# Performance work log

Measured on AMD Instinct MI355X. Metric: run time of the kernel, lower is better.

The kernel has to match this reference:

```python
import jax, jax.numpy as jnp
import numpy as np

BN_EPS = 1e-5


def _maxpool2(x):
    # x: [b, c, h, w] -> [b, c, h//2, w//2], 2x2 max pool, stride 2
    b, c, h, w = x.shape
    return x.reshape(b, c, h // 2, 2, w // 2, 2).max(axis=(3, 5))


def setup_inputs() -> dict:
    key = jax.random.key(0)
    ks = jax.random.split(key, 9)
    b, C, H, W = 8, 512, 64, 64
    Ci = C // 2  # inter_channels = 256
    return {
        "x": jax.random.normal(ks[0], (b, C, H, W), dtype=jnp.float32),
        "g_w": jax.random.normal(ks[1], (Ci, C), dtype=jnp.float32) * 0.02,
        "g_b": jax.random.normal(ks[2], (Ci,), dtype=jnp.float32) * 0.02,
        "W_w": jax.random.normal(ks[3], (C, Ci), dtype=jnp.float32) * 0.02,
        "W_b": jax.random.normal(ks[4], (C,), dtype=jnp.float32) * 0.02,
        "bn_gamma": jax.random.normal(ks[5], (C,), dtype=jnp.float32),
        "bn_beta": jax.random.normal(ks[6], (C,), dtype=jnp.float32),
        "bn_mean": jax.random.normal(ks[7], (C,), dtype=jnp.float32),
        "bn_var": jax.random.uniform(ks[8], (C,), dtype=jnp.float32, minval=0.5, maxval=1.5),
    }


def reference(x, g_w, g_b, W_w, W_b, bn_gamma, bn_beta, bn_mean, bn_var):
    b, C, H, W = x.shape
    Ci = g_w.shape[0]

    # g branch: conv1x1 (C -> Ci) then 2x2 maxpool, flatten to values [b, Nk, Ci]
    g_x = jnp.einsum('bchw,oc->bohw', x, g_w) + g_b[None, :, None, None]
    g_x = _maxpool2(g_x).reshape(b, Ci, -1).transpose(0, 2, 1)  # [b, Nk, Ci]

    # theta: identity, flattened queries [b, Nq, C]
    theta = x.reshape(b, C, -1).transpose(0, 2, 1)  # [b, Nq, C]
    # phi: identity + 2x2 maxpool, keys [b, C, Nk]
    phi = _maxpool2(x).reshape(b, C, -1)  # [b, C, Nk]

    # attention (unscaled dot product + softmax over keys)
    f = jnp.einsum('bnc,bck->bnk', theta, phi)  # [b, Nq, Nk]
    attn = jax.nn.softmax(f, axis=-1)
    y = jnp.einsum('bnk,bko->bno', attn, g_x)  # [b, Nq, Ci]
    y = y.transpose(0, 2, 1).reshape(b, Ci, H, W)

    # W: conv1x1 (Ci -> C) + BatchNorm2d (eval mode with running stats)
    W_y = jnp.einsum('bchw,oc->bohw', y, W_w) + W_b[None, :, None, None]
    inv_std = jax.lax.rsqrt(bn_var + BN_EPS)
    W_y = (W_y - bn_mean[None, :, None, None]) * (bn_gamma * inv_std)[None, :, None, None] \
          + bn_beta[None, :, None, None]

    return W_y + x
```

## Files before the change

kernel.cpp:

```cpp
#include <hip/hip_runtime.h>
#include <stdint.h>

typedef __attribute__((ext_vector_type(4))) float f32x4;
typedef __attribute__((ext_vector_type(8))) short short8_t;
typedef __attribute__((ext_vector_type(8))) unsigned short ushort8_t;

__device__ __forceinline__ unsigned short f2bf(float f) {
    unsigned int u = __builtin_bit_cast(unsigned int, f);
    u = (u + 0x7fffu + ((u >> 16) & 1u)) >> 16;
    return (unsigned short)u;
}
__device__ __forceinline__ float bf2f(unsigned short h) {
    unsigned int u = ((unsigned int)h) << 16;
    return __builtin_bit_cast(float, u);
}

__device__ __forceinline__ void gll16(const unsigned short* g, unsigned short* l) {
    __builtin_amdgcn_global_load_lds(
        (const __attribute__((address_space(1))) void*)g,
        (__attribute__((address_space(3))) void*)l, 16, 0, 0);
}

__global__ __launch_bounds__(256) void prep_w(
    const float* __restrict__ g_w, const float* __restrict__ W_w,
    const float* __restrict__ W_b, const float* __restrict__ gamma,
    const float* __restrict__ beta, const float* __restrict__ mean,
    const float* __restrict__ var,
    unsigned short* __restrict__ gwb, unsigned short* __restrict__ wwb,
    float* __restrict__ bnA, float* __restrict__ bnB)
{
    int i = blockIdx.x * 256 + threadIdx.x;
    if (i < 256 * 512) { gwb[i] = f2bf(g_w[i]); wwb[i] = f2bf(W_w[i]); }
    if (i < 512) {
        float is = rsqrtf(var[i] + 1e-5f);
        float a = gamma[i] * is;
        bnA[i] = a;
        bnB[i] = (W_b[i] - mean[i]) * a + beta[i];
    }
}

__global__ void build_q(const float* __restrict__ x, unsigned short* __restrict__ Qh)
{
    __shared__ float t[32][33];
    int b = blockIdx.z, p0 = blockIdx.x * 32, c0 = blockIdx.y * 32;
    const float* xb = x + (long)b * 512 * 4096;
    int tx = threadIdx.x, ty = threadIdx.y;
    for (int i = 0; i < 4; i++)
        t[ty + i * 8][tx] = xb[(long)(c0 + ty + i * 8) * 4096 + p0 + tx];
    __syncthreads();
    unsigned short* qb = Qh + (long)b * 4096 * 512;
    for (int i = 0; i < 4; i++) {
        float v = t[tx][ty + i * 8];
        long row = (long)(p0 + ty + i * 8) * 512;
        qb[row + c0 + tx] = f2bf(v);
    }
}

__global__ void build_k(const float* __restrict__ x, unsigned short* __restrict__ Kh)
{
    __shared__ float t[32][33];
    int b = blockIdx.z, k0 = blockIdx.x * 32, c0 = blockIdx.y * 32;
    const float* xb = x + (long)b * 512 * 4096;
    int tx = threadIdx.x, ty = threadIdx.y;
    for (int i = 0; i < 4; i++) {
        int c = c0 + ty + i * 8;
        int k = k0 + tx;
        int h = k >> 5, w = k & 31;
        const float* base = xb + (long)c * 4096 + h * 128 + w * 2;
        float v = fmaxf(fmaxf(base[0], base[1]), fmaxf(base[64], base[65]));
        t[ty + i * 8][tx] = v;
    }
    __syncthreads();
    unsigned short* kb = Kh + (long)b * 1024 * 512;
    for (int i = 0; i < 4; i++) {
        float v = t[tx][ty + i * 8];
        long row = (long)(k0 + ty + i * 8) * 512;
        kb[row + c0 + tx] = f2bf(v);
    }
}

__global__ __launch_bounds__(256) void build_v(
    const unsigned short* __restrict__ Gt, const float* __restrict__ g_b,
    unsigned short* __restrict__ Gp)
{
    int b = blockIdx.z;
    int k  = blockIdx.x * 32 + (threadIdx.x & 31);
    int ci = blockIdx.y * 8 + (threadIdx.x >> 5);
    int h = k >> 5, w = k & 31;
    const unsigned short* g = Gt + (long)b * 4096 * 256;
    long p = (long)(h * 128 + w * 2) * 256 + ci;
    float v0 = bf2f(g[p]),        v1 = bf2f(g[p + 256]);
    float v2 = bf2f(g[p + 64*256]), v3 = bf2f(g[p + 65*256]);
    float v = fmaxf(fmaxf(v0, v1), fmaxf(v2, v3)) + g_b[ci];
    Gp[(long)b * 256 * 1024 + (long)ci * 1024 + k] = f2bf(v);
}

__global__ __launch_bounds__(256) void pv_fused(
    const unsigned short* __restrict__ S, long sbstr,
    const unsigned short* __restrict__ Gp, long gbstr,
    unsigned short* __restrict__ Y, long ybstr)
{
    __shared__ unsigned short lV[256 * 64];
    __shared__ unsigned short lP[64 * 64];
    __shared__ float pm[256], pl[256];
    __shared__ float lm[64], li[64];

    const int tid = threadIdx.x;
    const int wid = tid >> 6, lane = tid & 63;

    unsigned gx = gridDim.x, gy = gridDim.y;
    unsigned nwg = gx * gy;
    unsigned lin = blockIdx.x + gx * blockIdx.y;
    unsigned l = ((nwg & 7u) == 0u) ? ((lin & 7u) * (nwg >> 3) + (lin >> 3)) : lin;
    unsigned bx = l % gx, by = l / gx;

    const int q0 = (int)bx * 64;
    const unsigned short* Sb = S + by * sbstr + (long)q0 * 1024;
    const unsigned short* Gb = Gp + by * gbstr;
    unsigned short* Yb = Y + by * ybstr + (long)q0 * 256;

    {
        int r = tid >> 2, qq = tid & 3;
        const unsigned short* p = Sb + (long)r * 1024 + qq * 256;
        float m = -3.0e38f, s = 0.f;
        for (int i = 0; i < 32; i++) {
            ushort8_t v = *(const ushort8_t*)(p + i * 8);
            float f0 = bf2f(v[0]), f1 = bf2f(v[1]), f2 = bf2f(v[2]), f3 = bf2f(v[3]);
            float f4 = bf2f(v[4]), f5 = bf2f(v[5]), f6 = bf2f(v[6]), f7 = bf2f(v[7]);
            float cm = fmaxf(fmaxf(fmaxf(f0, f1), fmaxf(f2, f3)),
                             fmaxf(fmaxf(f4, f5), fmaxf(f6, f7)));
            if (cm > m) { s *= __expf(m - cm); m = cm; }
            s += __expf(f0 - m) + __expf(f1 - m) + __expf(f2 - m) + __expf(f3 - m)
               + __expf(f4 - m) + __expf(f5 - m) + __expf(f6 - m) + __expf(f7 - m);
        }
        pm[tid] = m; pl[tid] = s;
    }
    __syncthreads();
    if (tid < 64) {
        float m0 = pm[tid*4], m1 = pm[tid*4+1], m2 = pm[tid*4+2], m3 = pm[tid*4+3];
        float m = fmaxf(fmaxf(m0, m1), fmaxf(m2, m3));
        float s = pl[tid*4]   * __expf(m0 - m) + pl[tid*4+1] * __expf(m1 - m)
                + pl[tid*4+2] * __expf(m2 - m) + pl[tid*4+3] * __expf(m3 - m);
        lm[tid] = m; li[tid] = 1.0f / s;
    }

    const int wr = wid >> 1, wc = wid & 1;
    const int lr = lane & 15, lg = lane >> 4;
    const int srA = lane >> 3;
    const int scg = (((lane & 7) ^ srA) << 3);
    const int pr = tid >> 2;
    const int pc = (tid & 3) * 2;

    f32x4 acc[2][8];
    for (int mi = 0; mi < 2; mi++)
        for (int ni = 0; ni < 8; ni++)
            acc[mi][ni] = (f32x4){0.f, 0.f, 0.f, 0.f};

    for (int kb = 0; kb < 16; kb++) {
        __syncthreads();
        for (int i = 0; i < 8; i++) {
            int cibase = i * 32 + wid * 8;
            gll16(Gb + (long)(cibase + srA) * 1024 + kb * 64 + scg, &lV[cibase * 64]);
        }
        {
            float m = lm[pr];
            const unsigned short* sp = Sb + (long)pr * 1024 + kb * 64 + pc * 8;
            for (int j = 0; j < 2; j++) {
                ushort8_t v = *(const ushort8_t*)(sp + j * 8);
                ushort8_t o8;
                for (int e = 0; e < 8; e++) o8[e] = f2bf(__expf(bf2f(v[e]) - m));
                int c = pc + j;
                *(ushort8_t*)(&lP[pr * 64 + ((c ^ (pr & 7)) * 8)]) = o8;
            }
        }
        __syncthreads();
        for (int ks = 0; ks < 2; ks++) {
            short8_t af[2], bfr[8];
            for (int mi = 0; mi < 2; mi++) {
                int row = wr * 32 + mi * 16 + lr;
                int ch = ((ks * 4 + lg) ^ (row & 7)) * 8;
                af[mi] = *(const short8_t*)(&lP[row * 64 + ch]);
            }
            for (int ni = 0; ni < 8; ni++) {
                int row = wc * 128 + ni * 16 + lr;
                int ch = ((ks * 4 + lg) ^ (row & 7)) * 8;
                bfr[ni] = *(const short8_t*)(&lV[row * 64 + ch]);
            }
            for (int mi = 0; mi < 2; mi++)
                for (int ni = 0; ni < 8; ni++)
                    acc[mi][ni] = __builtin_amdgcn_mfma_f32_16x16x32_bf16(
                        af[mi], bfr[ni], acc[mi][ni], 0, 0, 0);
        }
    }

    for (int mi = 0; mi < 2; mi++) {
        for (int ni = 0; ni < 8; ni++) {
            int ci = wc * 128 + ni * 16 + lr;
            int rbase = wr * 32 + mi * 16 + lg * 4;
            for (int r = 0; r < 4; r++) {
                int row = rbase + r;
                Yb[(long)row * 256 + ci] = f2bf(acc[mi][ni][r] * li[row]);
            }
        }
    }
}

template<int EPI, int AFOLD, int BFOLD>
__global__ __launch_bounds__(256) void gemm_abt(
    const unsigned short* __restrict__ A, int lda, long abstr,
    const unsigned short* __restrict__ B, int ldb, long bbstr,
    void* __restrict__ Cv, int ldc, long cbstr,
    int K,
    const float* __restrict__ bnA, const float* __restrict__ bnB,
    const float* __restrict__ Xres, long xbstr)
{
    __shared__ unsigned short lA[128 * 64];
    __shared__ unsigned short lB[128 * 64];
    const int tid = threadIdx.x;
    const int wid = tid >> 6, lane = tid & 63;

    unsigned gx = gridDim.x, gy = gridDim.y;
    unsigned nwg = gx * gy * gridDim.z;
    unsigned lin = blockIdx.x + gx * (blockIdx.y + gy * blockIdx.z);
    unsigned l = ((nwg & 7u) == 0u) ? ((lin & 7u) * (nwg >> 3) + (lin >> 3)) : lin;
    unsigned bx = l % gx;
    unsigned rem = l / gx;
    unsigned by = rem % gy;
    unsigned bz = rem / gy;

    const int z = (int)bz;
    const int m0 = (int)by * 128, n0 = (int)bx * 128;
    const unsigned short* Ab = A + z * abstr;
    const unsigned short* Bb = B + z * bbstr;
    const int wr = wid >> 1, wc = wid & 1;
    const int lr = lane & 15, lg = lane >> 4;

    const int srA = lane >> 3;
    const int scg = (((lane & 7) ^ srA) << 3);

    f32x4 acc[4][4];
    for (int mi = 0; mi < 4; mi++)
        for (int ni = 0; ni < 4; ni++)
            acc[mi][ni] = (f32x4){0.f, 0.f, 0.f, 0.f};

    for (int k0 = 0; k0 < K; k0 += 64) {
        int ak0 = (AFOLD && k0 >= AFOLD) ? k0 - AFOLD : k0;
        int bk0 = (BFOLD && k0 >= BFOLD) ? k0 - BFOLD : k0;
        __syncthreads();
        for (int i = 0; i < 4; i++) {
            int rowbase = i * 32 + wid * 8;
            gll16(Ab + (long)(m0 + rowbase + srA) * lda + ak0 + scg, &lA[rowbase * 64]);
            gll16(Bb + (long)(n0 + rowbase + srA) * ldb + bk0 + scg, &lB[rowbase * 64]);
        }
        __syncthreads();
        for (int kk = 0; kk < 2; kk++) {
            short8_t af[4], bfr[4];
            for (int mi = 0; mi < 4; mi++) {
                int row = wr * 64 + mi * 16 + lr;
                int ch = ((kk * 4 + lg) ^ (row & 7)) * 8;
                af[mi] = *(const short8_t*)(&lA[row * 64 + ch]);
            }
            for (int ni = 0; ni < 4; ni++) {
                int row = wc * 64 + ni * 16 + lr;
                int ch = ((kk * 4 + lg) ^ (row & 7)) * 8;
                bfr[ni] = *(const short8_t*)(&lB[row * 64 + ch]);
            }
            for (int mi = 0; mi < 4; mi++)
                for (int ni = 0; ni < 4; ni++)
                    acc[mi][ni] = __builtin_amdgcn_mfma_f32_16x16x32_bf16(
                        af[mi], bfr[ni], acc[mi][ni], 0, 0, 0);
        }
    }

    for (int mi = 0; mi < 4; mi++) {
        for (int ni = 0; ni < 4; ni++) {
            int ncol = n0 + wc * 64 + ni * 16 + lr;
            int mrow = m0 + wr * 64 + mi * 16 + lg * 4;
            for (int r = 0; r < 4; r++) {
                int row = mrow + r;
                float v = acc[mi][ni][r];
                long idx = z * cbstr + (long)row * ldc + ncol;
                if (EPI == 0) {
                    ((float*)Cv)[idx] = v;
                } else if (EPI == 1) {
                    ((unsigned short*)Cv)[idx] = f2bf(v);
                } else {
                    float o = v * bnA[row] + bnB[row] + Xres[z * xbstr + (long)row * ldc + ncol];
                    ((float*)Cv)[idx] = o;
                }
            }
        }
    }
}

__global__ void copy_residual(const float* __restrict__ x, float* __restrict__ out, long n)
{
    for (long i = blockIdx.x * 256ll + threadIdx.x; i < n; i += (long)gridDim.x * 256)
        out[i] = x[i];
}

extern "C" void kernel_launch(void* const* d_in, const int* in_sizes, int n_in,
                              void* d_out, int out_size, void* d_ws, size_t ws_size,
                              hipStream_t stream)
{
    const float* x     = (const float*)d_in[0];
    const float* g_w   = (const float*)d_in[1];
    const float* g_b   = (const float*)d_in[2];
    const float* W_w   = (const float*)d_in[3];
    const float* W_b   = (const float*)d_in[4];
    const float* gamma = (const float*)d_in[5];
    const float* beta  = (const float*)d_in[6];
    const float* mean  = (const float*)d_in[7];
    const float* var   = (const float*)d_in[8];
    float* out = (float*)d_out;

    char* ws = (char*)d_ws;
    size_t o = 0;
    auto alloc = [&](size_t bytes) { size_t r = o; o = (o + bytes + 255) & ~(size_t)255; return r; };
    size_t o_gwb = alloc(256 * 512 * 2);
    size_t o_wwb = alloc(512 * 256 * 2);
    size_t o_bnA = alloc(512 * 4);
    size_t o_bnB = alloc(512 * 4);
    size_t o_q   = alloc(8ull * 4096 * 512 * 2);
    size_t o_k   = alloc(8ull * 1024 * 512 * 2);
    size_t o_gp  = alloc(8ull * 256 * 1024 * 2);
    size_t o_y   = alloc(8ull * 4096 * 256 * 2);
    size_t o_s   = o;
    const size_t srow_bytes = 1024ull * 2;
    const size_t sb1 = 4096ull * srow_bytes;

    int G = 0, RC = 0;
    if      (o_s + 8 * sb1 <= ws_size) G = 8;
    else if (o_s + 4 * sb1 <= ws_size) G = 4;
    else if (o_s + 2 * sb1 <= ws_size) G = 2;
    else if (o_s + 1 * sb1 <= ws_size) G = 1;
    else {
        for (int rc = 2048; rc >= 128; rc >>= 1)
            if (o_s + (size_t)rc * srow_bytes <= ws_size) { RC = rc; break; }
        if (!RC) {
            copy_residual<<<dim3(2048), dim3(256), 0, stream>>>(x, out, (long)out_size);
            return;
        }
    }

    unsigned short* gwb = (unsigned short*)(ws + o_gwb);
    unsigned short* wwb = (unsigned short*)(ws + o_wwb);
    float* bnA = (float*)(ws + o_bnA);
    float* bnB = (float*)(ws + o_bnB);
    unsigned short* Qh  = (unsigned short*)(ws + o_q);
    unsigned short* Kh  = (unsigned short*)(ws + o_k);
    unsigned short* Gp  = (unsigned short*)(ws + o_gp);
    unsigned short* Y   = (unsigned short*)(ws + o_y);
    unsigned short* S   = (unsigned short*)(ws + o_s);

    prep_w<<<dim3(512), dim3(256), 0, stream>>>(g_w, W_w, W_b, gamma, beta, mean, var,
                                                gwb, wwb, bnA, bnB);
    build_q<<<dim3(128, 16, 8), dim3(32, 8), 0, stream>>>(x, Qh);
    build_k<<<dim3(32, 16, 8), dim3(32, 8), 0, stream>>>(x, Kh);

    gemm_abt<1, 0, 0><<<dim3(2, 32, 8), dim3(256), 0, stream>>>(
        Qh, 512, 4096l * 512,
        gwb, 512, 0,
        (void*)Y, 256, 4096l * 256, 512,
        nullptr, nullptr, nullptr, 0);

    build_v<<<dim3(32, 32, 8), dim3(256), 0, stream>>>(Y, g_b, Gp);

    if (G) {
        for (int bg = 0; bg < 8; bg += G) {
            gemm_abt<1, 0, 0><<<dim3(8, 32, G), dim3(256), 0, stream>>>(
                Qh + (size_t)bg * 4096 * 512, 512, 4096l * 512,
                Kh + (size_t)bg * 1024 * 512, 512, 1024l * 512,
                (void*)S, 1024, 4096l * 1024, 512,
                nullptr, nullptr, nullptr, 0);
            pv_fused<<<dim3(64, G), dim3(256), 0, stream>>>(
                S, 4096l * 1024,
                Gp + (size_t)bg * 256 * 1024, 256l * 1024,
                Y + (size_t)bg * 4096 * 256, 4096l * 256);
        }
    } else {
        for (int b = 0; b < 8; b++) {
            for (int r0 = 0; r0 < 4096; r0 += RC) {
                const unsigned short* Aq = Qh + (size_t)b * 4096 * 512 + (size_t)r0 * 512;
                gemm_abt<1, 0, 0><<<dim3(8, RC / 128, 1), dim3(256), 0, stream>>>(
                    Aq, 512, 0,
                    Kh + (size_t)b * 1024 * 512, 512, 0,
                    (void*)S, 1024, 0, 512,
                    nullptr, nullptr, nullptr, 0);
                pv_fused<<<dim3(RC / 64, 1), dim3(256), 0, stream>>>(
                    S, 0,
                    Gp + (size_t)b * 256 * 1024, 0,
                    Y + ((size_t)b * 4096 + r0) * 256, 0);
            }
        }
    }

    gemm_abt<2, 0, 0><<<dim3(32, 4, 8), dim3(256), 0, stream>>>(
        wwb, 256, 0,
        Y, 256, 4096l * 256,
        (void*)out, 4096, 512l * 4096, 256,
        bnA, bnB, x, 512l * 4096);
}
```

Measured before the change: 195.2 us.

## Compute softmax row max in QK GEMM epilogue and fuse Q/K build kernels

The QK^T GEMM epilogue now writes per-tile row maxima (16 partials per row) to a workspace buffer. pv_fused reduces these to get the row max and accumulates the softmax denominator during its exp pass, which removes the separate full read of S for online max/sum statistics. build_q and build_k are merged into one kernel so x is read once for both the transpose and the pooled keys. The cost is an extra small buffer, some epilogue shuffles in the GEMM, and a shuffle reduction at the end of pv_fused.

```diff
diff --git a/kernel.cpp b/kernel.cpp
--- a/kernel.cpp
+++ b/kernel.cpp
@@ -39,43 +39,35 @@
     }
 }
 
-__global__ void build_q(const float* __restrict__ x, unsigned short* __restrict__ Qh)
-{
-    __shared__ float t[32][33];
-    int b = blockIdx.z, p0 = blockIdx.x * 32, c0 = blockIdx.y * 32;
+__global__ __launch_bounds__(256) void build_qk(
+    const float* __restrict__ x, unsigned short* __restrict__ Qh,
+    unsigned short* __restrict__ Kh)
+{
+    __shared__ float t[32][129];
+    int b = blockIdx.z;
+    int p0 = blockIdx.x * 128, c0 = blockIdx.y * 32;
     const float* xb = x + (long)b * 512 * 4096;
-    int tx = threadIdx.x, ty = threadIdx.y;
-    for (int i = 0; i < 4; i++)
-        t[ty + i * 8][tx] = xb[(long)(c0 + ty + i * 8) * 4096 + p0 + tx];
+    int tid = threadIdx.x;
+    for (int i = 0; i < 16; i++) {
+        int idx = i * 256 + tid;
+        int c = idx >> 7, p = idx & 127;
+        t[c][p] = xb[(long)(c0 + c) * 4096 + p0 + p];
+    }
     __syncthreads();
     unsigned short* qb = Qh + (long)b * 4096 * 512;
+    for (int i = 0; i < 16; i++) {
+        int idx = i * 256 + tid;
+        int p = idx >> 5, c = idx & 31;
+        qb[(long)(p0 + p) * 512 + c0 + c] = f2bf(t[c][p]);
+    }
+    unsigned short* kb = Kh + (long)b * 1024 * 512;
+    int kp0 = p0 >> 2;
     for (int i = 0; i < 4; i++) {
-        float v = t[tx][ty + i * 8];
-        long row = (long)(p0 + ty + i * 8) * 512;
-        qb[row + c0 + tx] = f2bf(v);
-    }
-}
-
-__global__ void build_k(const float* __restrict__ x, unsigned short* __restrict__ Kh)
-{
-    __shared__ float t[32][33];
-    int b = blockIdx.z, k0 = blockIdx.x * 32, c0 = blockIdx.y * 32;
-    const float* xb = x + (long)b * 512 * 4096;
-    int tx = threadIdx.x, ty = threadIdx.y;
-    for (int i = 0; i < 4; i++) {
-        int c = c0 + ty + i * 8;
-        int k = k0 + tx;
-        int h = k >> 5, w = k & 31;
-        const float* base = xb + (long)c * 4096 + h * 128 + w * 2;
-        float v = fmaxf(fmaxf(base[0], base[1]), fmaxf(base[64], base[65]));
-        t[ty + i * 8][tx] = v;
-    }
-    __syncthreads();
-    unsigned short* kb = Kh + (long)b * 1024 * 512;
-    for (int i = 0; i < 4; i++) {
-        float v = t[tx][ty + i * 8];
-        long row = (long)(k0 + ty + i * 8) * 512;
-        kb[row + c0 + tx] = f2bf(v);
+        int idx = i * 256 + tid;
+        int w = idx >> 5, c = idx & 31;
+        float v = fmaxf(fmaxf(t[c][2 * w], t[c][2 * w + 1]),
+                        fmaxf(t[c][64 + 2 * w], t[c][64 + 2 * w + 1]));
+        kb[(long)(kp0 + w) * 512 + c0 + c] = f2bf(v);
     }
 }
 
@@ -97,12 +89,12 @@
 
 __global__ __launch_bounds__(256) void pv_fused(
     const unsigned short* __restrict__ S, long sbstr,
+    const float* __restrict__ Mrow, long mbstr,
     const unsigned short* __restrict__ Gp, long gbstr,
     unsigned short* __restrict__ Y, long ybstr)
 {
     __shared__ unsigned short lV[256 * 64];
     __shared__ unsigned short lP[64 * 64];
-    __shared__ float pm[256], pl[256];
     __shared__ float lm[64], li[64];
 
     const int tid = threadIdx.x;
@@ -119,29 +111,11 @@
     const unsigned short* Gb = Gp + by * gbstr;
     unsigned short* Yb = Y + by * ybstr + (long)q0 * 256;
 
-    {
-        int r = tid >> 2, qq = tid & 3;
-        const unsigned short* p = Sb + (long)r * 1024 + qq * 256;
-        float m = -3.0e38f, s = 0.f;
-        for (int i = 0; i < 32; i++) {
-            ushort8_t v = *(const ushort8_t*)(p + i * 8);
-            float f0 = bf2f(v[0]), f1 = bf2f(v[1]), f2 = bf2f(v[2]), f3 = bf2f(v[3]);
-            float f4 = bf2f(v[4]), f5 = bf2f(v[5]), f6 = bf2f(v[6]), f7 = bf2f(v[7]);
-            float cm = fmaxf(fmaxf(fmaxf(f0, f1), fmaxf(f2, f3)),
-                             fmaxf(fmaxf(f4, f5), fmaxf(f6, f7)));
-            if (cm > m) { s *= __expf(m - cm); m = cm; }
-            s += __expf(f0 - m) + __expf(f1 - m) + __expf(f2 - m) + __expf(f3 - m)
-               + __expf(f4 - m) + __expf(f5 - m) + __expf(f6 - m) + __expf(f7 - m);
-        }
-        pm[tid] = m; pl[tid] = s;
-    }
-    __syncthreads();
     if (tid < 64) {
-        float m0 = pm[tid*4], m1 = pm[tid*4+1], m2 = pm[tid*4+2], m3 = pm[tid*4+3];
-        float m = fmaxf(fmaxf(m0, m1), fmaxf(m2, m3));
-        float s = pl[tid*4]   * __expf(m0 - m) + pl[tid*4+1] * __expf(m1 - m)
-                + pl[tid*4+2] * __expf(m2 - m) + pl[tid*4+3] * __expf(m3 - m);
-        lm[tid] = m; li[tid] = 1.0f / s;
+        const float* mr = Mrow + by * mbstr + (long)(q0 + tid) * 16;
+        float m = mr[0];
+        for (int j = 1; j < 16; j++) m = fmaxf(m, mr[j]);
+        lm[tid] = m;
     }
 
     const int wr = wid >> 1, wc = wid & 1;
@@ -155,6 +129,7 @@
     for (int mi = 0; mi < 2; mi++)
         for (int ni = 0; ni < 8; ni++)
             acc[mi][ni] = (f32x4){0.f, 0.f, 0.f, 0.f};
+    float psum = 0.f;
 
     for (int kb = 0; kb < 16; kb++) {
         __syncthreads();
@@ -168,7 +143,11 @@
             for (int j = 0; j < 2; j++) {
                 ushort8_t v = *(const ushort8_t*)(sp + j * 8);
                 ushort8_t o8;
-                for (int e = 0; e < 8; e++) o8[e] = f2bf(__expf(bf2f(v[e]) - m));
+                for (int e = 0; e < 8; e++) {
+                    float pe = __expf(bf2f(v[e]) - m);
+                    psum += pe;
+                    o8[e] = f2bf(pe);
+                }
                 int c = pc + j;
                 *(ushort8_t*)(&lP[pr * 64 + ((c ^ (pr & 7)) * 8)]) = o8;
             }
@@ -193,6 +172,11 @@
         }
     }
 
+    psum += __shfl_xor(psum, 1);
+    psum += __shfl_xor(psum, 2);
+    if ((tid & 3) == 0) li[pr] = 1.0f / psum;
+    __syncthreads();
+
     for (int mi = 0; mi < 2; mi++) {
         for (int ni = 0; ni < 8; ni++) {
             int ci = wc * 128 + ni * 16 + lr;
@@ -205,14 +189,15 @@
     }
 }
 
-template<int EPI, int AFOLD, int BFOLD>
+template<int EPI, int ROWMAX>
 __global__ __launch_bounds__(256) void gemm_abt(
     const unsigned short* __restrict__ A, int lda, long abstr,
     const unsigned short* __restrict__ B, int ldb, long bbstr,
     void* __restrict__ Cv, int ldc, long cbstr,
     int K,
     const float* __restrict__ bnA, const float* __restrict__ bnB,
-    const float* __restrict__ Xres, long xbstr)
+    const float* __restrict__ Xres, long xbstr,
+    float* __restrict__ Mrow, long mbstr)
 {
     __shared__ unsigned short lA[128 * 64];
     __shared__ unsigned short lB[128 * 64];
@@ -244,13 +229,11 @@
             acc[mi][ni] = (f32x4){0.f, 0.f, 0.f, 0.f};
 
     for (int k0 = 0; k0 < K; k0 += 64) {
-        int ak0 = (AFOLD && k0 >= AFOLD) ? k0 - AFOLD : k0;
-        int bk0 = (BFOLD && k0 >= BFOLD) ? k0 - BFOLD : k0;
         __syncthreads();
         for (int i = 0; i < 4; i++) {
             int rowbase = i * 32 + wid * 8;
-            gll16(Ab + (long)(m0 + rowbase + srA) * lda + ak0 + scg, &lA[rowbase * 64]);
-            gll16(Bb + (long)(n0 + rowbase + srA) * ldb + bk0 + scg, &lB[rowbase * 64]);
+            gll16(Ab + (long)(m0 + rowbase + srA) * lda + k0 + scg, &lA[rowbase * 64]);
+            gll16(Bb + (long)(n0 + rowbase + srA) * ldb + k0 + scg, &lB[rowbase * 64]);
         }
         __syncthreads();
         for (int kk = 0; kk < 2; kk++) {
@@ -269,6 +252,23 @@
                 for (int ni = 0; ni < 4; ni++)
                     acc[mi][ni] = __builtin_amdgcn_mfma_f32_16x16x32_bf16(
                         af[mi], bfr[ni], acc[mi][ni], 0, 0, 0);
+        }
+    }
+
+    if (ROWMAX) {
+        for (int mi = 0; mi < 4; mi++) {
+            for (int r = 0; r < 4; r++) {
+                float mx = fmaxf(fmaxf(acc[mi][0][r], acc[mi][1][r]),
+                                 fmaxf(acc[mi][2][r], acc[mi][3][r]));
+                mx = fmaxf(mx, __shfl_xor(mx, 1));
+                mx = fmaxf(mx, __shfl_xor(mx, 2));
+                mx = fmaxf(mx, __shfl_xor(mx, 4));
+                mx = fmaxf(mx, __shfl_xor(mx, 8));
+                if (lr == 0) {
+                    int row = m0 + wr * 64 + mi * 16 + lg * 4 + r;
+                    Mrow[z * mbstr + (long)row * 16 + bx * 2 + wc] = mx;
+                }
+            }
         }
     }
 
@@ -325,6 +325,7 @@
     size_t o_k   = alloc(8ull * 1024 * 512 * 2);
     size_t o_gp  = alloc(8ull * 256 * 1024 * 2);
     size_t o_y   = alloc(8ull * 4096 * 256 * 2);
+    size_t o_m   = alloc(8ull * 4096 * 16 * 4);
     size_t o_s   = o;
     const size_t srow_bytes = 1024ull * 2;
     const size_t sb1 = 4096ull * srow_bytes;
@@ -351,30 +352,32 @@
     unsigned short* Kh  = (unsigned short*)(ws + o_k);
     unsigned short* Gp  = (unsigned short*)(ws + o_gp);
     unsigned short* Y   = (unsigned short*)(ws + o_y);
+    float* Mrow         = (float*)(ws + o_m);
     unsigned short* S   = (unsigned short*)(ws + o_s);
 
     prep_w<<<dim3(512), dim3(256), 0, stream>>>(g_w, W_w, W_b, gamma, beta, mean, var,
                                                 gwb, wwb, bnA, bnB);
-    build_q<<<dim3(128, 16, 8), dim3(32, 8), 0, stream>>>(x, Qh);
-    build_k<<<dim3(32, 16, 8), dim3(32, 8), 0, stream>>>(x, Kh);
-
-    gemm_abt<1, 0, 0><<<dim3(2, 32, 8), dim3(256), 0, stream>>>(
+    build_qk<<<dim3(32, 16, 8), dim3(256), 0, stream>>>(x, Qh, Kh);
+
+    gemm_abt<1, 0><<<dim3(2, 32, 8), dim3(256), 0, stream>>>(
         Qh, 512, 4096l * 512,
         gwb, 512, 0,
         (void*)Y, 256, 4096l * 256, 512,
-        nullptr, nullptr, nullptr, 0);
+        nullptr, nullptr, nullptr, 0, nullptr, 0);
 
     build_v<<<dim3(32, 32, 8), dim3(256), 0, stream>>>(Y, g_b, Gp);
 
     if (G) {
         for (int bg = 0; bg < 8; bg += G) {
-            gemm_abt<1, 0, 0><<<dim3(8, 32, G), dim3(256), 0, stream>>>(
+            gemm_abt<1, 1><<<dim3(8, 32, G), dim3(256), 0, stream>>>(
                 Qh + (size_t)bg * 4096 * 512, 512, 4096l * 512,
                 Kh + (size_t)bg * 1024 * 512, 512, 1024l * 512,
                 (void*)S, 1024, 4096l * 1024, 512,
-                nullptr, nullptr, nullptr, 0);
+                nullptr, nullptr, nullptr, 0,
+                Mrow + (size_t)bg * 4096 * 16, 4096l * 16);
             pv_fused<<<dim3(64, G), dim3(256), 0, stream>>>(
                 S, 4096l * 1024,
+                Mrow + (size_t)bg * 4096 * 16, 4096l * 16,
                 Gp + (size_t)bg * 256 * 1024, 256l * 1024,
                 Y + (size_t)bg * 4096 * 256, 4096l * 256);
         }
@@ -382,22 +385,25 @@
         for (int b = 0; b < 8; b++) {
             for (int r0 = 0; r0 < 4096; r0 += RC) {
                 const unsigned short* Aq = Qh + (size_t)b * 4096 * 512 + (size_t)r0 * 512;
-                gemm_abt<1, 0, 0><<<dim3(8, RC / 128, 1), dim3(256), 0, stream>>>(
+                gemm_abt<1, 1><<<dim3(8, RC / 128, 1), dim3(256), 0, stream>>>(
                     Aq, 512, 0,
                     Kh + (size_t)b * 1024 * 512, 512, 0,
                     (void*)S, 1024, 0, 512,
-                    nullptr, nullptr, nullptr, 0);
+                    nullptr, nullptr, nullptr, 0,
+                    Mrow, 0);
                 pv_fused<<<dim3(RC / 64, 1), dim3(256), 0, stream>>>(
                     S, 0,
+                    Mrow, 0,
                     Gp + (size_t)b * 256 * 1024, 0,
                     Y + ((size_t)b * 4096 + r0) * 256, 0);
             }
         }
     }
 
-    gemm_abt<2, 0, 0><<<dim3(32, 4, 8), dim3(256), 0, stream>>>(
+    gemm_abt<2, 0><<<dim3(32, 4, 8), dim3(256), 0, stream>>>(
         wwb, 256, 0,
         Y, 256, 4096l * 256,
         (void*)out, 4096, 512l * 4096, 256,
-        bnA, bnB, x, 512l * 4096);
-}
+        bnA, bnB, x, 512l * 4096,
+        nullptr, 0);
+}
```

New measurement: 183.0 us. 6.3% less time.
